# Kernel tuning notes

Hardware: AMD Instinct MI355X
Metric: run time of the kernel (lower is better)

## Reference

```python
import jax, jax.numpy as jnp
import numpy as np
import math

# ---- config (YOLOv3 / 416, COCO) ----
ANCS_SCALE = np.array([[0.024,0.031],[0.038,0.072],[0.079,0.055],
                       [0.072,0.147],[0.149,0.108],[0.142,0.286],
                       [0.279,0.216],[0.375,0.476],[0.897,0.784]], dtype=np.float32)
NUMS_CENG = [2704, 676, 169]          # 52^2, 26^2, 13^2
NUMS_ANC = [3, 3, 3]
NUM_CLASSES = 80
LOSS_WEIGHT = [1.0, 1.0, 1.0]
B, NGT = 32, 20
HWA = sum(NUMS_CENG) * 3              # 10647
GDIM = 1 + NUM_CLASSES + 4 + 1 + 4    # conf + cls + txywh + weight + ltrb
FP16_EPS = 0.0009765625               # torch.finfo(float16).eps
BCE_EPS = 1e-6
GRIDS = [int(math.sqrt(n)) for n in NUMS_CENG]          # [52, 26, 13]
OFFS = [int(x) for x in np.cumsum([0] + NUMS_CENG)[:3]]  # layer offsets in cells


def ltrb2xywh(b):
    return jnp.concatenate([(b[..., :2] + b[..., 2:]) * 0.5, b[..., 2:] - b[..., :2]], axis=-1)


def x_bce(p, g):
    p = jnp.clip(p, BCE_EPS, 1.0 - BCE_EPS)
    return -(g * jnp.log(p) + (1.0 - g) * jnp.log(1.0 - p))


def fmatch4yolov3(gb_ltrb, glabels):
    """gb_ltrb [NGT,4] float, glabels [NGT] int -> g_yolo_one [HWA,GDIM].
    Faithful to the torch code, including the (buggy) inner loop over ALL
    GTs' best-anchor ids for each GT i, and the write order (-1 ignore first,
    positive row overwrite after), replicated via a sequential lax.scan."""
    ancs = jnp.asarray(ANCS_SCALE)
    gxywh = ltrb2xywh(gb_ltrb)
    wh = gxywh[:, 2:]                                     # [NGT,2]
    # wh-only IoU (boxes concentric at origin)
    inter = jnp.minimum(wh[:, None, 0], ancs[None, :, 0]) * jnp.minimum(wh[:, None, 1], ancs[None, :, 1])
    union = wh.prod(-1)[:, None] + ancs.prod(-1)[None, :] - inter
    ids_p_anc = jnp.argmax(inter / union, axis=-1).astype(jnp.int32)  # [NGT]
    weights = 2.0 - wh.prod(-1)
    onehot = jax.nn.one_hot(glabels - 1, NUM_CLASSES, dtype=gb_ltrb.dtype)
    g0 = jnp.zeros((HWA, GDIM), dtype=gb_ltrb.dtype)
    neg = jnp.full((3, 1), -1.0, dtype=gb_ltrb.dtype)

    def step(g, p):
        i = p // NGT            # GT whose cxy / wh / label are used
        k = p % NGT             # GT whose best anchor id is used
        cxy = gxywh[i, :2]
        a = ids_p_anc[k]
        ceng = a // NUMS_ANC[0]
        for j in range(3):      # static loop over the 3 layers
            grid, off = GRIDS[j], OFFS[j]
            colrow = (cxy * grid).astype(jnp.int32)       # [col,row]
            idx = (off + colrow[1] * grid + colrow[0]) * 3
            # ignore: conf=-1 for all 3 anchors of this cell
            g = jax.lax.dynamic_update_slice(g, neg, (idx, 0))
            # candidate positive row for this layer
            txy = (cxy - colrow.astype(cxy.dtype) / grid) * grid
            twh = jnp.log(wh[i] / ancs[a])
            t = jnp.concatenate([jnp.ones((1,), cxy.dtype), onehot[i], txy, twh,
                                 weights[i][None], gb_ltrb[i]])     # [GDIM]
            pidx = idx + (a % NUMS_ANC[j])
            cur = jax.lax.dynamic_slice(g, (pidx, 0), (1, GDIM))
            g = jax.lax.dynamic_update_slice(g, jnp.where(ceng == j, t[None, :], cur), (pidx, 0))
        return g, None

    g, _ = jax.lax.scan(step, g0, jnp.arange(NGT * NGT, dtype=jnp.int32))
    return g


def _forward(pconf, pcls, ptxywh, gboxes_ltrb, glabels):
    gyolos = jax.lax.stop_gradient(jax.vmap(fmatch4yolov3)(gboxes_ltrb, glabels))  # [B,HWA,GDIM]
    s_ = 1 + NUM_CLASSES
    gconf = gyolos[:, :, 0]
    mask_pos = (gconf > 0).astype(pconf.dtype)
    mask_neg = (gconf == 0).astype(pconf.dtype)
    nums_pos = jnp.clip(mask_pos.sum(-1), FP16_EPS, None)
    # cls loss (BCE on sigmoid, pos cells only)
    lv = x_bce(jax.nn.sigmoid(pcls), gyolos[:, :, 1:s_])
    l_cls = ((lv.sum(-1) * mask_pos).sum(-1) / nums_pos).mean() * LOSS_WEIGHT[2]
    # conf loss (MSE on sigmoid, masked means)
    pconf_sig = jax.nn.sigmoid(pconf).reshape(pconf.shape[0], -1)
    lv = (pconf_sig - gconf) ** 2
    l_conf_pos = (lv * mask_pos).sum() / mask_pos.sum() * LOSS_WEIGHT[0] * 30
    l_conf_neg = (lv * mask_neg).sum() / mask_neg.sum() * LOSS_WEIGHT[1] * 30
    # box loss: xy BCE, wh MSE, weighted by (2 - w*h)
    weight = gyolos[:, :, s_ + 4]
    lv = x_bce(jax.nn.sigmoid(ptxywh[:, :, :2]), gyolos[:, :, s_:s_ + 2])
    l_txty = ((lv.sum(-1) * mask_pos * weight).sum(-1) / nums_pos).mean()
    lv = (ptxywh[:, :, 2:4] - gyolos[:, :, s_ + 2:s_ + 4]) ** 2
    l_twth = ((lv.sum(-1) * mask_pos * weight).sum(-1) / nums_pos).mean()
    return l_conf_pos + l_conf_neg + l_cls + l_txty + l_twth


def setup_inputs() -> dict:
    key = jax.random.key(0)
    k1, k2, k3, k4, k5, k6 = jax.random.split(key, 6)
    pconf = jax.random.normal(k1, (B, HWA, 1), dtype=jnp.float32)
    pcls = jax.random.normal(k2, (B, HWA, NUM_CLASSES), dtype=jnp.float32)
    ptxywh = jax.random.normal(k3, (B, HWA, 4), dtype=jnp.float32)
    cxy = jax.random.uniform(k4, (B, NGT, 2), minval=0.2, maxval=0.8)
    wh = jax.random.uniform(k5, (B, NGT, 2), minval=0.05, maxval=0.3)
    gboxes_ltrb = jnp.concatenate([cxy - wh * 0.5, cxy + wh * 0.5], axis=-1)
    glabels = jax.random.randint(k6, (B, NGT), 1, NUM_CLASSES + 1, dtype=jnp.int32)
    return {"pconf": pconf, "pcls": pcls, "ptxywh": ptxywh,
            "gboxes_ltrb": gboxes_ltrb, "glabels": glabels}


def reference(pconf, pcls, ptxywh, gboxes_ltrb, glabels):
    return _forward(pconf, pcls, ptxywh, gboxes_ltrb, glabels)
```

## Files before the change

kernel.cpp:

```cpp
#include <hip/hip_runtime.h>
#include <math.h>

#define BATCH 32
#define NGT 20
#define HWA 10647
#define NCLS 80
#define FP16_EPS 0.0009765625f
#define BCE_EPS 1e-6f

__device__ __constant__ float ANCS[9][2] = {
    {0.024f, 0.031f}, {0.038f, 0.072f}, {0.079f, 0.055f},
    {0.072f, 0.147f}, {0.149f, 0.108f}, {0.142f, 0.286f},
    {0.279f, 0.216f}, {0.375f, 0.476f}, {0.897f, 0.784f}};

__device__ __forceinline__ float fexp(float x) { return __expf(x); }
__device__ __forceinline__ float flog(float x) { return __logf(x); }
__device__ __forceinline__ float fsig(float x) {
  return __builtin_amdgcn_rcpf(1.0f + __expf(-x));
}


__global__ __launch_bounds__(256) void yolo_main(
    const float* __restrict__ pconf,
    const float* __restrict__ pcls,
    const float* __restrict__ ptxywh,
    const float* __restrict__ gbox,
    const int* __restrict__ glab,
    float* __restrict__ part)
{
  const int b = blockIdx.x;
  const int tid = threadIdx.x;

  __shared__ int cell[HWA];
  __shared__ int pos_list[256];
  __shared__ float s_cx[NGT], s_cy[NGT], s_w[NGT], s_h[NGT], s_wt[NGT];
  __shared__ int s_a[NGT], s_lab[NGT], s_idx[NGT][3];
  __shared__ int s_np;
  __shared__ float red[4][8];

  for (int r = tid; r < HWA; r += 256) cell[r] = 0;
  if (tid == 0) s_np = 0;
  if (tid < NGT) {
    const float* gb = gbox + (b * NGT + tid) * 4;
    float l = gb[0], t = gb[1], r = gb[2], bo = gb[3];
    float cx = (l + r) * 0.5f, cy = (t + bo) * 0.5f;
    float w = r - l, h = bo - t;
    s_cx[tid] = cx; s_cy[tid] = cy; s_w[tid] = w; s_h[tid] = h;
    s_wt[tid] = 2.0f - w * h;
    s_lab[tid] = glab[b * NGT + tid];
    float best = -1e30f; int bi = 0;
    for (int a = 0; a < 9; ++a) {
      float inter = fminf(w, ANCS[a][0]) * fminf(h, ANCS[a][1]);
      float uni = w * h + ANCS[a][0] * ANCS[a][1] - inter;
      float ratio = inter / uni;
      if (ratio > best) { best = ratio; bi = a; }
    }
    s_a[tid] = bi;
    const int GR[3] = {52, 26, 13};
    const int OF[3] = {0, 2704, 3380};
    for (int j = 0; j < 3; ++j) {
      int col = (int)(cx * (float)GR[j]);
      int row = (int)(cy * (float)GR[j]);
      s_idx[tid][j] = (OF[j] + row * GR[j] + col) * 3;
    }
  }
  __syncthreads();

  for (int p = tid; p < NGT * NGT; p += 256) {
    int i = p / NGT, k = p - i * NGT;
    int a = s_a[k];
    int ceng = a / 3;
    int pn = (2 * p + 1) << 16;
    int pp = ((2 * p + 2) << 16) | (1 << 15) | (i * 9 + a);
    for (int j = 0; j < 3; ++j) {
      int idx = s_idx[i][j];
      atomicMax(&cell[idx], pn);
      atomicMax(&cell[idx + 1], pn);
      atomicMax(&cell[idx + 2], pn);
      if (ceng == j) atomicMax(&cell[idx + (a - ceng * 3)], pp);
    }
  }
  __syncthreads();

  float sum_pos = 0.f, sum_neg = 0.f;
  int cnt_pos = 0, cnt_neg = 0;
  for (int r = tid; r < HWA; r += 256) {
    int c = cell[r];
    float x = pconf[(size_t)b * HWA + r];
    float s = fsig(x);
    if (c == 0) {
      sum_neg += s * s; cnt_neg++;
    } else if (c & (1 << 15)) {
      float d = s - 1.0f; sum_pos += d * d; cnt_pos++;
      int slot = atomicAdd(&s_np, 1);
      if (slot < 256) pos_list[slot] = ((c & 0xFF) << 16) | r;
    }
  }
  __syncthreads();
  int P = s_np;

  float cls_sum = 0.f;
  for (int idx = tid; idx < P * NCLS; idx += 256) {
    int pr = idx / NCLS, c = idx - pr * NCLS;
    int pk = pos_list[pr];
    int r = pk & 0xFFFF, rec = pk >> 16;
    int i = rec / 9;
    int lab = s_lab[i] - 1;
    float x = pcls[((size_t)b * HWA + r) * NCLS + c];
    float s = fsig(x);
    s = fminf(fmaxf(s, BCE_EPS), 1.0f - BCE_EPS);
    float g = (c == lab) ? 1.0f : 0.0f;
    cls_sum += -(g * flog(s) + (1.0f - g) * flog(1.0f - s));
  }

  float txty_sum = 0.f, twth_sum = 0.f;
  for (int q = tid; q < P; q += 256) {
    int pk = pos_list[q];
    int r = pk & 0xFFFF, rec = pk >> 16;
    int i = rec / 9, a = rec - i * 9;
    int ceng = a / 3;
    const int GR[3] = {52, 26, 13};
    float grid = (float)GR[ceng];
    float cx = s_cx[i], cy = s_cy[i];
    int col = (int)(cx * grid), row = (int)(cy * grid);
    float tx = (cx - (float)col / grid) * grid;
    float ty = (cy - (float)row / grid) * grid;
    float twx = flog(s_w[i] / ANCS[a][0]);
    float twy = flog(s_h[i] / ANCS[a][1]);
    float wgt = s_wt[i];
    const float* pt = ptxywh + ((size_t)b * HWA + r) * 4;
    float s0 = fsig(pt[0]);
    float s1 = fsig(pt[1]);
    s0 = fminf(fmaxf(s0, BCE_EPS), 1.0f - BCE_EPS);
    s1 = fminf(fmaxf(s1, BCE_EPS), 1.0f - BCE_EPS);
    float b0 = -(tx * flog(s0) + (1.0f - tx) * flog(1.0f - s0));
    float b1 = -(ty * flog(s1) + (1.0f - ty) * flog(1.0f - s1));
    txty_sum += (b0 + b1) * wgt;
    float d2 = pt[2] - twx, d3 = pt[3] - twy;
    twth_sum += (d2 * d2 + d3 * d3) * wgt;
  }

  float v[7] = {sum_pos, sum_neg, cls_sum, txty_sum, twth_sum,
                (float)cnt_pos, (float)cnt_neg};
  int lane = tid & 63, wv = tid >> 6;
  for (int m = 0; m < 7; ++m) {
    float x = v[m];
    for (int o = 32; o > 0; o >>= 1) x += __shfl_down(x, o, 64);
    if (lane == 0) red[wv][m] = x;
  }
  __syncthreads();
  if (tid == 0) {
    float* w = part + b * 8;
    for (int m = 0; m < 7; ++m)
      w[m] = red[0][m] + red[1][m] + red[2][m] + red[3][m];
  }
}

__global__ void yolo_final(const float* __restrict__ part,
                           float* __restrict__ out) {
  int t = threadIdx.x;
  float sp = 0, sn = 0, cp = 0, cn = 0, lc = 0, lt = 0, lw = 0;
  if (t < BATCH) {
    const float* w = part + t * 8;
    sp = w[0]; sn = w[1]; cp = w[5]; cn = w[6];
    float np = fmaxf(w[5], FP16_EPS);
    float rnp = 1.0f / np;
    lc = w[2] * rnp; lt = w[3] * rnp; lw = w[4] * rnp;
  }
  for (int o = 32; o > 0; o >>= 1) {
    sp += __shfl_down(sp, o, 64);
    sn += __shfl_down(sn, o, 64);
    cp += __shfl_down(cp, o, 64);
    cn += __shfl_down(cn, o, 64);
    lc += __shfl_down(lc, o, 64);
    lt += __shfl_down(lt, o, 64);
    lw += __shfl_down(lw, o, 64);
  }
  if (t == 0) {
    out[0] = sp / cp * 30.0f + sn / cn * 30.0f +
             (lc + lt + lw) * (1.0f / (float)BATCH);
  }
}

extern "C" void kernel_launch(void* const* d_in, const int* in_sizes, int n_in,
                              void* d_out, int out_size, void* d_ws,
                              size_t ws_size, hipStream_t stream) {
  const float* pconf  = (const float*)d_in[0];
  const float* pcls   = (const float*)d_in[1];
  const float* ptxywh = (const float*)d_in[2];
  const float* gbox   = (const float*)d_in[3];
  const int*   glab   = (const int*)d_in[4];
  float* part = (float*)d_ws;

  yolo_main<<<BATCH, 256, 0, stream>>>(pconf, pcls, ptxywh, gbox, glab, part);
  yolo_final<<<1, 64, 0, stream>>>(part, (float*)d_out);
}
```

Before: 171.9 us.

## Split per-batch cell scan across 8 slice blocks per image

Launches a 2D grid of batch by 8 slices so each block scans only a slice of the anchor cells, raising parallelism from 32 blocks to 256 on a GPU with many CUs. Each block still redoes the GT matching and cell-map setup redundantly. The final reduction now first sums the 8 per-slice partials per image, then forms the per-image normalized losses before summing over the batch. The pos_list cap of 256 is now applied per slice.

```diff
diff --git a/kernel.cpp b/kernel.cpp
--- a/kernel.cpp
+++ b/kernel.cpp
@@ -2,6 +2,8 @@
 #include <math.h>
 
 #define BATCH 32
+#define NSLICE 8
+#define SLICE_LEN 1331
 #define NGT 20
 #define HWA 10647
 #define NCLS 80
@@ -13,7 +15,6 @@
     {0.072f, 0.147f}, {0.149f, 0.108f}, {0.142f, 0.286f},
     {0.279f, 0.216f}, {0.375f, 0.476f}, {0.897f, 0.784f}};
 
-__device__ __forceinline__ float fexp(float x) { return __expf(x); }
 __device__ __forceinline__ float flog(float x) { return __logf(x); }
 __device__ __forceinline__ float fsig(float x) {
   return __builtin_amdgcn_rcpf(1.0f + __expf(-x));
@@ -29,6 +30,7 @@
     float* __restrict__ part)
 {
   const int b = blockIdx.x;
+  const int sl = blockIdx.y;
   const int tid = threadIdx.x;
 
   __shared__ int cell[HWA];
@@ -82,9 +84,11 @@
   }
   __syncthreads();
 
+  const int r0 = sl * SLICE_LEN;
+  const int r1 = min(r0 + SLICE_LEN, HWA);
   float sum_pos = 0.f, sum_neg = 0.f;
   int cnt_pos = 0, cnt_neg = 0;
-  for (int r = tid; r < HWA; r += 256) {
+  for (int r = r0 + tid; r < r1; r += 256) {
     int c = cell[r];
     float x = pconf[(size_t)b * HWA + r];
     float s = fsig(x);
@@ -150,35 +154,49 @@
   }
   __syncthreads();
   if (tid == 0) {
-    float* w = part + b * 8;
+    float* w = part + (b * NSLICE + sl) * 8;
     for (int m = 0; m < 7; ++m)
       w[m] = red[0][m] + red[1][m] + red[2][m] + red[3][m];
   }
 }
 
-__global__ void yolo_final(const float* __restrict__ part,
-                           float* __restrict__ out) {
-  int t = threadIdx.x;
-  float sp = 0, sn = 0, cp = 0, cn = 0, lc = 0, lt = 0, lw = 0;
-  if (t < BATCH) {
-    const float* w = part + t * 8;
-    sp = w[0]; sn = w[1]; cp = w[5]; cn = w[6];
-    float np = fmaxf(w[5], FP16_EPS);
+__global__ __launch_bounds__(256) void yolo_final(
+    const float* __restrict__ part, float* __restrict__ out) {
+  const int t = threadIdx.x;
+  __shared__ float sb[BATCH][8];
+  float v[7];
+  const float* w = part + t * 8;
+#pragma unroll
+  for (int m = 0; m < 7; ++m) v[m] = w[m];
+#pragma unroll
+  for (int o = 4; o > 0; o >>= 1)
+#pragma unroll
+    for (int m = 0; m < 7; ++m) v[m] += __shfl_down(v[m], o, 8);
+  if ((t & 7) == 0) {
+    int b = t >> 3;
+    float np = fmaxf(v[5], FP16_EPS);
     float rnp = 1.0f / np;
-    lc = w[2] * rnp; lt = w[3] * rnp; lw = w[4] * rnp;
-  }
-  for (int o = 32; o > 0; o >>= 1) {
-    sp += __shfl_down(sp, o, 64);
-    sn += __shfl_down(sn, o, 64);
-    cp += __shfl_down(cp, o, 64);
-    cn += __shfl_down(cn, o, 64);
-    lc += __shfl_down(lc, o, 64);
-    lt += __shfl_down(lt, o, 64);
-    lw += __shfl_down(lw, o, 64);
-  }
-  if (t == 0) {
-    out[0] = sp / cp * 30.0f + sn / cn * 30.0f +
-             (lc + lt + lw) * (1.0f / (float)BATCH);
+    sb[b][0] = v[0];
+    sb[b][1] = v[1];
+    sb[b][2] = v[5];
+    sb[b][3] = v[6];
+    sb[b][4] = v[2] * rnp;
+    sb[b][5] = v[3] * rnp;
+    sb[b][6] = v[4] * rnp;
+  }
+  __syncthreads();
+  if (t < 32) {
+    float u[7];
+#pragma unroll
+    for (int m = 0; m < 7; ++m) u[m] = sb[t][m];
+#pragma unroll
+    for (int o = 16; o > 0; o >>= 1)
+#pragma unroll
+      for (int m = 0; m < 7; ++m) u[m] += __shfl_down(u[m], o, 32);
+    if (t == 0) {
+      out[0] = u[0] / u[2] * 30.0f + u[1] / u[3] * 30.0f +
+               (u[4] + u[5] + u[6]) * (1.0f / (float)BATCH);
+    }
   }
 }
 
@@ -192,6 +210,7 @@
   const int*   glab   = (const int*)d_in[4];
   float* part = (float*)d_ws;
 
-  yolo_main<<<BATCH, 256, 0, stream>>>(pconf, pcls, ptxywh, gbox, glab, part);
-  yolo_final<<<1, 64, 0, stream>>>(part, (float*)d_out);
-}
+  dim3 grid(BATCH, NSLICE);
+  yolo_main<<<grid, 256, 0, stream>>>(pconf, pcls, ptxywh, gbox, glab, part);
+  yolo_final<<<1, 256, 0, stream>>>(part, (float*)d_out);
+}
```

Measured after the change: 155.1 us. 9.8% less time.
